# Kernel optimization log

Hardware: AMD Instinct MI355X
Metric: run time of the kernel (lower is better)

The kernel has to match this reference:

```python
import jax, jax.numpy as jnp
import numpy as np

N = 8192
K = 64
EPS = 1e-7
BN_EPS = 1e-5


def _norm(x):
    return jnp.sqrt(jnp.sum(x * x, axis=-1, keepdims=True))


def _bn(x, gamma, beta):
    # BatchNorm2d in training mode (batch statistics, biased variance)
    mu = jnp.mean(x, axis=(0, 2, 3), keepdims=True)
    var = jnp.mean((x - mu) ** 2, axis=(0, 2, 3), keepdims=True)
    return gamma.reshape(1, -1, 1, 1) * (x - mu) / jnp.sqrt(var + BN_EPS) + beta.reshape(1, -1, 1, 1)


def _conv1x1(x, w, b):
    # 1x1 conv == per-pixel linear: x [B,C,H,W], w [O,C]
    return jnp.einsum('bchw,oc->bohw', x, w) + b.reshape(1, -1, 1, 1)


def setup_inputs() -> dict:
    key = jax.random.key(0)
    ks = jax.random.split(key, 24)
    d = {}
    d['points'] = jax.random.normal(ks[0], (1, N, 3), jnp.float32)
    # graph_conv weights (torch code re-draws these every forward; here fixed params)
    lim0 = float(np.sqrt(6.0 / (4 + 64)))
    d['gw0'] = jax.random.uniform(ks[1], (4, 64), jnp.float32, -lim0, lim0)
    lim = float(np.sqrt(6.0 / (64 + 64)))
    for i in range(1, 5):
        d[f'gw{i}'] = jax.random.uniform(ks[1 + i], (64, 64), jnp.float32, -lim, lim)
    # mlp_1: 4->64->128, mlp_2: 192->256->1024 (1x1 convs + BN)
    d['c1w'] = jax.random.normal(ks[6], (64, 4), jnp.float32) * 0.1
    d['c1b'] = jnp.zeros((64,), jnp.float32)
    d['bn1g'] = jnp.ones((64,), jnp.float32)
    d['bn1b'] = jnp.zeros((64,), jnp.float32)
    d['c2w'] = jax.random.normal(ks[7], (128, 64), jnp.float32) * 0.1
    d['c2b'] = jnp.zeros((128,), jnp.float32)
    d['bn2g'] = jnp.ones((128,), jnp.float32)
    d['bn2b'] = jnp.zeros((128,), jnp.float32)
    d['c3w'] = jax.random.normal(ks[8], (256, 192), jnp.float32) * 0.05
    d['c3b'] = jnp.zeros((256,), jnp.float32)
    d['bn3g'] = jnp.ones((256,), jnp.float32)
    d['bn3b'] = jnp.zeros((256,), jnp.float32)
    d['c4w'] = jax.random.normal(ks[9], (1024, 256), jnp.float32) * 0.05
    d['c4b'] = jnp.zeros((1024,), jnp.float32)
    d['bn4g'] = jnp.ones((1024,), jnp.float32)
    d['bn4b'] = jnp.zeros((1024,), jnp.float32)
    return d


def _knn_search(points, k):
    # pairwise squared distances via ||a||^2 - 2ab + ||b||^2
    r = jnp.sum(points * points, axis=-1, keepdims=True)          # [1,N,1]
    dis = r - 2.0 * jnp.einsum('bnd,bmd->bnm', points, points) + jnp.swapaxes(r, 1, 2)
    _, idx = jax.lax.top_k(-dis, k)                                # [1,N,K]
    knn_pts = jax.vmap(lambda p, i: p[i])(points, idx)             # [1,N,K,3]
    return knn_pts


def _proj_knn(knn_pts):
    b, n, k, _ = knn_pts.shape
    pc = knn_pts - knn_pts[:, :, :1, :]                            # center on first neighbor (self)
    vn = jnp.sqrt(jnp.sum(pc * pc, axis=-1))                       # [1,N,K]
    id1 = jnp.argmax(vn, axis=-1)                                  # farthest neighbor
    a1 = jnp.take_along_axis(pc, jnp.broadcast_to(id1[:, :, None, None], (b, n, 1, 3)), axis=2)[:, :, 0, :]
    a1 = a1 / (_norm(a1) + EPS)
    a2 = jnp.mean(pc, axis=2)
    a2 = a2 / (_norm(a2) + EPS)
    a3 = a1 + 1.5 * a2
    a3 = a3 / (_norm(a3) + EPS)
    den = _norm(pc) + EPS                                          # [1,N,K,1]
    f1 = jnp.sum(pc * a1[:, :, None, :], axis=-1, keepdims=True) / den
    f2 = jnp.sum(pc * a2[:, :, None, :], axis=-1, keepdims=True) / den
    f3 = jnp.sum(pc * a3[:, :, None, :], axis=-1, keepdims=True) / den
    return jnp.concatenate([f1, f2, f3, vn[..., None]], axis=-1)   # [1,N,K,4]


def _proj_points(points):
    b, n, _ = points.shape
    vn = jnp.sqrt(jnp.sum(points * points, axis=-1))               # [1,N]
    i1 = jnp.argmax(vn, axis=-1)
    i2 = jnp.argmin(vn, axis=-1)
    a1 = jnp.take_along_axis(points, jnp.broadcast_to(i1[:, None, None], (b, 1, 3)), axis=1)[:, 0, :]
    a1 = a1 / (_norm(a1) + EPS)
    a2 = jnp.take_along_axis(points, jnp.broadcast_to(i2[:, None, None], (b, 1, 3)), axis=1)[:, 0, :]
    a2 = a2 / (_norm(a2) + EPS)
    a3 = a1 + 1.5 * a2
    a3 = a3 / (_norm(a3) + EPS)
    den = _norm(points) + EPS                                      # [1,N,1]
    f1 = jnp.sum(points * a1[:, None, :], axis=-1, keepdims=True) / den
    f2 = jnp.sum(points * a2[:, None, :], axis=-1, keepdims=True) / den
    f3 = jnp.sum(points * a3[:, None, :], axis=-1, keepdims=True) / den
    return jnp.concatenate([f1, f2, f3, vn[..., None]], axis=-1)   # [1,N,4]


def reference(points, gw0, gw1, gw2, gw3, gw4,
              c1w, c1b, bn1g, bn1b, c2w, c2b, bn2g, bn2b,
              c3w, c3b, bn3g, bn3b, c4w, c4b, bn4g, bn4b):
    n = points.shape[1]
    # upper branch: KNN -> rotation-invariant local feats -> 5-layer MLP -> max over K
    knn_pts = _knn_search(points, K)
    feat_up = _proj_knn(knn_pts)                                   # [1,N,K,4]
    x = feat_up.reshape(-1, 4)
    for w in (gw0, gw1, gw2, gw3, gw4):
        x = jax.nn.relu(x @ w)
    x = x.reshape(1, n, K, 64)
    emb_up = jnp.max(x, axis=2, keepdims=True)                     # [1,N,1,64]
    emb_up = emb_up.reshape(1, 64, n, 1)                           # raw view (reshape), as in torch
    # lower branch: global rotation-invariant feats -> mlp_1
    feat_down = _proj_points(points)                               # [1,N,4]
    emb_down = feat_down.reshape(1, 4, n, 1)                       # raw view (reshape), as in torch
    h = jax.nn.relu(_bn(_conv1x1(emb_down, c1w, c1b), bn1g, bn1b))
    h = jax.nn.relu(_bn(_conv1x1(h, c2w, c2b), bn2g, bn2b))        # [1,128,N,1]
    emb = jnp.concatenate([emb_up, h], axis=1)                     # [1,192,N,1]
    out = jax.nn.relu(_bn(_conv1x1(emb, c3w, c3b), bn3g, bn3b))
    out = jax.nn.relu(_bn(_conv1x1(out, c4w, c4b), bn4g, bn4b))    # [1,1024,N,1]
    return out
```

## Files before the change

kernel.cpp:

```cpp
#include <hip/hip_runtime.h>
#include <hip/hip_bf16.h>

#define NPTS 8192
#define KNN 64
#define EPSF 1e-7f

#define OFF_P4      0
#define OFF_STATS   32768
#define OFF_AVEC    36000
#define OFF_PART    36012
#define OFF_FEATDN  36864
#define OFF_WT1     69632
#define OFF_GWT     69888
#define OFF_BW2     79104
#define OFF_BW3     83200
#define OFF_BW4     107776
#define OFF_XB1     238848
#define OFF_XB3     500992
#define OFF_XB4     1287424
#define OFF_Y1      2336000
#define OFF_Y2      2860288
#define OFF_Y3      3908864
#define OFF_FEATUP  6006016

typedef __bf16 bf16x8 __attribute__((ext_vector_type(8)));
typedef float  f32x4  __attribute__((ext_vector_type(4)));

__device__ __forceinline__ unsigned f2u(float f) {
    unsigned u = __float_as_uint(f);
    return ((int)u >= 0) ? (u | 0x80000000u) : ~u;
}
__device__ __forceinline__ float key_to_f(unsigned long long k) {
    unsigned v = (unsigned)(k >> 32);
    unsigned ob = (v & 0x80000000u) ? (v ^ 0x80000000u) : ~v;
    return __uint_as_float(ob);
}
__device__ __forceinline__ unsigned short f2bf(float x) {
    unsigned u = __float_as_uint(x);
    unsigned r = (u + 0x7FFFu + ((u >> 16) & 1u)) >> 16;
    return (unsigned short)r;
}
__device__ __forceinline__ unsigned long long u64min(unsigned long long a, unsigned long long b){ return a < b ? a : b; }
__device__ __forceinline__ unsigned long long u64max(unsigned long long a, unsigned long long b){ return a < b ? b : a; }

__device__ __forceinline__ unsigned long long sort_merge(
    unsigned long long key, unsigned long long cur, int lane)
{
    #pragma unroll
    for (int k = 2; k <= 64; k <<= 1) {
        #pragma unroll
        for (int j = k >> 1; j > 0; j >>= 1) {
            unsigned long long o = __shfl_xor(key, j);
            bool up = ((lane & k) == 0);
            bool lower = ((lane & j) == 0);
            key = (lower == up) ? u64min(key, o) : u64max(key, o);
        }
    }
    unsigned long long rev = __shfl(key, 63 - lane);
    unsigned long long m = u64min(cur, rev);
    #pragma unroll
    for (int j = 32; j > 0; j >>= 1) {
        unsigned long long o = __shfl_xor(m, j);
        m = ((lane & j) == 0) ? u64min(m, o) : u64max(m, o);
    }
    return m;
}

__global__ __launch_bounds__(256) void prep_a_kernel(
    const float* __restrict__ points, float* __restrict__ ws)
{
    const int n = blockIdx.x * 256 + threadIdx.x;
    float x = points[3*n+0], y = points[3*n+1], z = points[3*n+2];
    float rr = x*x + y*y + z*z;
    ((float4*)(ws + OFF_P4))[n] = make_float4(x, y, z, rr);
    float vn = sqrtf(rr);
    unsigned b = __float_as_uint(vn);
    unsigned long long mxk = ((unsigned long long)b << 32) | (unsigned long long)(0xFFFFFFFFu - (unsigned)n);
    unsigned long long mnk = ((unsigned long long)b << 32) | (unsigned long long)(unsigned)n;
    for (int j = 32; j > 0; j >>= 1) {
        mxk = u64max(mxk, __shfl_xor(mxk, j));
        mnk = u64min(mnk, __shfl_xor(mnk, j));
    }
    __shared__ unsigned long long smx[4], smn[4];
    int wid = threadIdx.x >> 6;
    if ((threadIdx.x & 63) == 0) { smx[wid] = mxk; smn[wid] = mnk; }
    __syncthreads();
    if (threadIdx.x == 0) {
        unsigned long long MX = 0ull, MN = ~0ull;
        for (int i = 0; i < 4; ++i) { MX = u64max(MX, smx[i]); MN = u64min(MN, smn[i]); }
        unsigned long long* parts = (unsigned long long*)(ws + OFF_PART);
        parts[2*blockIdx.x + 0] = MX;
        parts[2*blockIdx.x + 1] = MN;
    }
}

__global__ __launch_bounds__(64) void prep_b_kernel(
    const float* __restrict__ points, float* __restrict__ ws)
{
    const int lane = threadIdx.x;
    const unsigned long long* parts = (const unsigned long long*)(ws + OFF_PART);
    unsigned long long mxk = (lane < 32) ? parts[2*lane + 0] : 0ull;
    unsigned long long mnk = (lane < 32) ? parts[2*lane + 1] : ~0ull;
    for (int j = 32; j > 0; j >>= 1) {
        mxk = u64max(mxk, __shfl_xor(mxk, j));
        mnk = u64min(mnk, __shfl_xor(mnk, j));
    }
    if (lane == 0) {
        int i1 = (int)(0xFFFFFFFFu - (unsigned)(mxk & 0xFFFFFFFFu));
        int i2 = (int)(unsigned)(mnk & 0xFFFFFFFFu);
        float a1x = points[3*i1+0], a1y = points[3*i1+1], a1z = points[3*i1+2];
        float n1 = sqrtf(a1x*a1x + a1y*a1y + a1z*a1z) + EPSF;
        a1x /= n1; a1y /= n1; a1z /= n1;
        float a2x = points[3*i2+0], a2y = points[3*i2+1], a2z = points[3*i2+2];
        float n2 = sqrtf(a2x*a2x + a2y*a2y + a2z*a2z) + EPSF;
        a2x /= n2; a2y /= n2; a2z /= n2;
        float a3x = a1x + 1.5f*a2x, a3y = a1y + 1.5f*a2y, a3z = a1z + 1.5f*a2z;
        float n3 = sqrtf(a3x*a3x + a3y*a3y + a3z*a3z) + EPSF;
        a3x /= n3; a3y /= n3; a3z /= n3;
        float* av = ws + OFF_AVEC;
        av[0]=a1x; av[1]=a1y; av[2]=a1z;
        av[3]=a2x; av[4]=a2y; av[5]=a2z;
        av[6]=a3x; av[7]=a3y; av[8]=a3z;
    }
}

__global__ __launch_bounds__(256) void prep_c_kernel(float* __restrict__ ws)
{
    const int n = blockIdx.x * 256 + threadIdx.x;
    const float* av = ws + OFF_AVEC;
    float4 v = ((const float4*)(ws + OFF_P4))[n];
    float vn = sqrtf(v.w);
    float den = vn + EPSF;
    float f1 = (v.x*av[0] + v.y*av[1] + v.z*av[2]) / den;
    float f2 = (v.x*av[3] + v.y*av[4] + v.z*av[5]) / den;
    float f3 = (v.x*av[6] + v.y*av[7] + v.z*av[8]) / den;
    float4* f4 = (float4*)(ws + OFF_FEATDN + 4*n);
    *f4 = make_float4(f1, f2, f3, vn);
}

__global__ __launch_bounds__(256) void wt_kernel(
    const float* __restrict__ c1w, const float* __restrict__ c2w,
    const float* __restrict__ c3w, const float* __restrict__ c4w,
    const float* __restrict__ gw0, const float* __restrict__ gw1,
    const float* __restrict__ gw2, const float* __restrict__ gw3,
    const float* __restrict__ gw4,
    float* __restrict__ ws)
{
    const int t = blockIdx.x * 256 + threadIdx.x;
    const int T = gridDim.x * 256;
    for (int m = t; m < 2944; m += T) ws[OFF_STATS + m] = 0.f;
    for (int m = t; m < 64*4; m += T) { int o = m >> 2, c = m & 3; ws[OFF_WT1 + c*64 + o] = c1w[m]; }

    unsigned short* bw2 = (unsigned short*)(ws + OFF_BW2);
    for (int m = t; m < 128*64; m += T)   bw2[m] = f2bf(c2w[m]);
    unsigned short* bw3 = (unsigned short*)(ws + OFF_BW3);
    for (int m = t; m < 256*192; m += T)  bw3[m] = f2bf(c3w[m]);
    unsigned short* bw4 = (unsigned short*)(ws + OFF_BW4);
    for (int m = t; m < 1024*256; m += T) bw4[m] = f2bf(c4w[m]);

    unsigned short* gwt = (unsigned short*)(ws + OFF_GWT);
    for (int m = t; m < 2048; m += T) {
        int o = m >> 5, i = m & 31;
        gwt[m] = (i < 4) ? f2bf(gw0[i*64 + o]) : (unsigned short)0;
    }
    const float* gsrc[4] = {gw1, gw2, gw3, gw4};
    for (int l = 0; l < 4; ++l) {
        const float* g = gsrc[l];
        unsigned short* dst = gwt + 2048 + l*4096;
        for (int m = t; m < 4096; m += T) { int o = m >> 6, i = m & 63; dst[m] = f2bf(g[i*64 + o]); }
    }
}

__global__ __launch_bounds__(512) void knn_feat_kernel(
    const float4* __restrict__ p4, float4* __restrict__ feat_up)
{
    __shared__ __align__(16) float4 scand[2048];
    __shared__ unsigned long long queue[8][128];
    const int lane = threadIdx.x & 63;
    const int wid  = threadIdx.x >> 6;
    const int q = blockIdx.x * 8 + wid;

    const float4 qa = p4[q];
    unsigned long long cur = ~0ull;
    float kthd = __builtin_inff();
    int qc = 0;
    unsigned long long* Q = queue[wid];

    for (int base = 0; base < NPTS; base += 2048) {
        __syncthreads();
        for (int t = threadIdx.x; t < 2048; t += 512) scand[t] = p4[base + t];
        __syncthreads();
        #pragma unroll 2
        for (int sub = 0; sub < 2048; sub += 64) {
            float4 cd = scand[sub + lane];
            float dot = fmaf(qa.x, cd.x, fmaf(qa.y, cd.y, qa.z * cd.z));
            float d   = fmaf(-2.f, dot, qa.w) + cd.w;
            bool p = d < kthd;
            unsigned long long m = __ballot(p);
            if (m) {
                int prefix = __builtin_amdgcn_mbcnt_hi((unsigned)(m >> 32),
                              __builtin_amdgcn_mbcnt_lo((unsigned)m, 0));
                if (p) Q[qc + prefix] = ((unsigned long long)f2u(d) << 32)
                                      | (unsigned long long)(unsigned)(base + sub + lane);
                qc += __popcll(m);
                if (qc >= 64) {
                    qc -= 64;
                    cur = sort_merge(Q[qc + lane], cur, lane);
                    kthd = key_to_f(__shfl(cur, 63));
                }
            }
        }
    }
    cur = sort_merge((lane < qc) ? Q[lane] : ~0ull, cur, lane);

    int nidx = (int)(unsigned)(cur & 0xFFFFFFFFu);
    float4 np = p4[nidx];
    float ox = __shfl(np.x, 0), oy = __shfl(np.y, 0), oz = __shfl(np.z, 0);
    float pcx = np.x - ox, pcy = np.y - oy, pcz = np.z - oz;
    float vn = sqrtf(pcx*pcx + pcy*pcy + pcz*pcz);

    unsigned long long ak = ((unsigned long long)__float_as_uint(vn) << 32)
                          | (unsigned long long)(unsigned)(63 - lane);
    for (int s = 32; s > 0; s >>= 1) ak = u64max(ak, __shfl_xor(ak, s));
    int id1 = 63 - (int)(unsigned)(ak & 0xFFFFFFFFu);

    float a1x = __shfl(pcx, id1), a1y = __shfl(pcy, id1), a1z = __shfl(pcz, id1);
    float n1 = sqrtf(a1x*a1x + a1y*a1y + a1z*a1z) + EPSF;
    a1x /= n1; a1y /= n1; a1z /= n1;

    float sx = pcx, sy = pcy, sz = pcz;
    for (int s = 32; s > 0; s >>= 1) {
        sx += __shfl_xor(sx, s); sy += __shfl_xor(sy, s); sz += __shfl_xor(sz, s);
    }
    float a2x = sx * (1.f/64.f), a2y = sy * (1.f/64.f), a2z = sz * (1.f/64.f);
    float n2 = sqrtf(a2x*a2x + a2y*a2y + a2z*a2z) + EPSF;
    a2x /= n2; a2y /= n2; a2z /= n2;

    float a3x = a1x + 1.5f*a2x, a3y = a1y + 1.5f*a2y, a3z = a1z + 1.5f*a2z;
    float n3 = sqrtf(a3x*a3x + a3y*a3y + a3z*a3z) + EPSF;
    a3x /= n3; a3y /= n3; a3z /= n3;

    float den = vn + EPSF;
    float f1 = (pcx*a1x + pcy*a1y + pcz*a1z) / den;
    float f2 = (pcx*a2x + pcy*a2y + pcz*a2z) / den;
    float f3 = (pcx*a3x + pcy*a3y + pcz*a3z) / den;
    feat_up[q*64 + lane] = make_float4(f1, f2, f3, vn);
}

#define BROW 72
__global__ __launch_bounds__(256) void mlp_kernel(
    const float4* __restrict__ feat_up,
    const unsigned short* __restrict__ gwt,
    unsigned short* __restrict__ xb3)
{
    __shared__ __align__(16) unsigned short Blds[4][64 * BROW];
    const int lane = threadIdx.x & 63;
    const int wid  = threadIdx.x >> 6;
    const int q = blockIdx.x * 4 + wid;
    const int c = lane & 15, g = lane >> 4;
    unsigned short* B = Blds[wid];

    {
        float4 f = feat_up[q*64 + lane];
        uint2 p0;
        p0.x = (unsigned)f2bf(f.x) | ((unsigned)f2bf(f.y) << 16);
        p0.y = (unsigned)f2bf(f.z) | ((unsigned)f2bf(f.w) << 16);
        *(uint2*)&B[lane*BROW] = p0;
        *(uint2*)&B[lane*BROW + 4] = make_uint2(0, 0);
        uint4 z4 = make_uint4(0, 0, 0, 0);
        *(uint4*)&B[lane*BROW + 8]  = z4;
        *(uint4*)&B[lane*BROW + 16] = z4;
        *(uint4*)&B[lane*BROW + 24] = z4;
    }

    const unsigned short* Wl[5] = {gwt, gwt + 2048, gwt + 6144, gwt + 10240, gwt + 14336};
    f32x4 acc[4][4];

    for (int layer = 0; layer < 5; ++layer) {
        const int wstride = (layer == 0) ? 32 : 64;
        const int nks = (layer == 0) ? 1 : 2;
        #pragma unroll
        for (int mb = 0; mb < 4; ++mb)
            #pragma unroll
            for (int nb = 0; nb < 4; ++nb)
                acc[mb][nb] = (f32x4){0.f, 0.f, 0.f, 0.f};

        for (int ks = 0; ks < nks; ++ks) {
            bf16x8 af[4], bf[4];
            #pragma unroll
            for (int mb = 0; mb < 4; ++mb)
                af[mb] = *(const bf16x8*)(Wl[layer] + (mb*16 + c)*wstride + ks*32 + g*8);
            #pragma unroll
            for (int nb = 0; nb < 4; ++nb)
                bf[nb] = *(const bf16x8*)&B[(nb*16 + c)*BROW + ks*32 + g*8];
            #pragma unroll
            for (int mb = 0; mb < 4; ++mb)
                #pragma unroll
                for (int nb = 0; nb < 4; ++nb)
                    acc[mb][nb] = __builtin_amdgcn_mfma_f32_16x16x32_bf16(af[mb], bf[nb], acc[mb][nb], 0, 0, 0);
        }

        if (layer < 4) {
            #pragma unroll
            for (int mb = 0; mb < 4; ++mb) {
                #pragma unroll
                for (int nb = 0; nb < 4; ++nb) {
                    f32x4 a = acc[mb][nb];
                    float r0 = fmaxf(a[0], 0.f), r1 = fmaxf(a[1], 0.f);
                    float r2 = fmaxf(a[2], 0.f), r3 = fmaxf(a[3], 0.f);
                    uint2 pw;
                    pw.x = (unsigned)f2bf(r0) | ((unsigned)f2bf(r1) << 16);
                    pw.y = (unsigned)f2bf(r2) | ((unsigned)f2bf(r3) << 16);
                    *(uint2*)&B[(nb*16 + c)*BROW + mb*16 + g*4] = pw;
                }
            }
        }
    }

    const int cc = q >> 7;
    const int pbase = (q & 127) << 6;
    #pragma unroll
    for (int mb = 0; mb < 4; ++mb) {
        float v[4];
        #pragma unroll
        for (int r = 0; r < 4; ++r)
            v[r] = fmaxf(fmaxf(fmaxf(acc[mb][0][r], acc[mb][1][r]),
                               fmaxf(acc[mb][2][r], acc[mb][3][r])), 0.f);
        #pragma unroll
        for (int mask = 1; mask <= 8; mask <<= 1)
            #pragma unroll
            for (int r = 0; r < 4; ++r)
                v[r] = fmaxf(v[r], __shfl_xor(v[r], mask));
        if (c == 0) {
            #pragma unroll
            for (int r = 0; r < 4; ++r) {
                const int f = mb*16 + g*4 + r;
                xb3[(size_t)(pbase + f) * 192 + cc] = f2bf(v[r]);
            }
        }
    }
}

__global__ __launch_bounds__(256) void conv1_kernel(
    const float* __restrict__ x, const float* __restrict__ wt,
    const float* __restrict__ bias, float* __restrict__ y,
    float* __restrict__ stout)
{
    const int tid = threadIdx.x;
    const int p  = blockIdx.x * 256 + tid;
    const int o0 = blockIdx.y * 32;
    float acc[32];
    #pragma unroll
    for (int u = 0; u < 32; ++u) acc[u] = bias[o0 + u];
    #pragma unroll
    for (int c = 0; c < 4; ++c) {
        float xv = x[c * NPTS + p];
        const float* wr = wt + c * 64 + o0;
        #pragma unroll
        for (int u = 0; u < 32; ++u) acc[u] = fmaf(xv, wr[u], acc[u]);
    }
    #pragma unroll
    for (int u = 0; u < 32; ++u) y[(o0 + u) * NPTS + p] = acc[u];

    __shared__ float ps[4][32], pss[4][32];
    const int wid = tid >> 6, lane = tid & 63;
    #pragma unroll
    for (int u = 0; u < 32; ++u) {
        float s = acc[u], ss = acc[u] * acc[u];
        for (int j = 32; j > 0; j >>= 1) { s += __shfl_xor(s, j); ss += __shfl_xor(ss, j); }
        if (lane == 0) { ps[wid][u] = s; pss[wid][u] = ss; }
    }
    __syncthreads();
    if (tid < 32) {
        float S  = ps[0][tid] + ps[1][tid] + ps[2][tid] + ps[3][tid];
        float SS = pss[0][tid] + pss[1][tid] + pss[2][tid] + pss[3][tid];
        atomicAdd(&stout[o0 + tid], S);
        atomicAdd(&stout[64 + o0 + tid], SS);
    }
}

__global__ __launch_bounds__(256) void bnpack_kernel(
    const float* __restrict__ y, const float* __restrict__ st,
    const float* __restrict__ gam, const float* __restrict__ bet,
    int C, int stride, int coff, unsigned short* __restrict__ xb)
{
    __shared__ float sc[256], sh[256];
    __shared__ __align__(16) unsigned short tile[64][264];
    const int tid = threadIdx.x;
    for (int cc = tid; cc < C; cc += 256) {
        float mu  = st[cc] * (1.f / 8192.f);
        float var = st[C + cc] * (1.f / 8192.f) - mu * mu;
        float s = gam[cc] / sqrtf(var + 1e-5f);
        sc[cc] = s; sh[cc] = bet[cc] - mu * s;
    }
    __syncthreads();
    const int pl = tid & 63, g = tid >> 6;
    const int p = blockIdx.x * 64 + pl;
    for (int c0 = g * 8; c0 < C; c0 += 32) {
        unsigned pk[4];
        #pragma unroll
        for (int h = 0; h < 4; ++h) {
            float v0 = fmaxf(fmaf(y[(c0 + 2*h    ) * NPTS + p], sc[c0 + 2*h    ], sh[c0 + 2*h    ]), 0.f);
            float v1 = fmaxf(fmaf(y[(c0 + 2*h + 1) * NPTS + p], sc[c0 + 2*h + 1], sh[c0 + 2*h + 1]), 0.f);
            pk[h] = (unsigned)f2bf(v0) | ((unsigned)f2bf(v1) << 16);
        }
        *(uint4*)&tile[pl][c0] = make_uint4(pk[0], pk[1], pk[2], pk[3]);
    }
    __syncthreads();
    const int cpr = C >> 3;
    const int nch = 64 * cpr;
    for (int idx = tid; idx < nch; idx += 256) {
        int r = idx / cpr, cc = (idx - r * cpr) * 8;
        *(uint4*)&xb[(size_t)(blockIdx.x * 64 + r) * stride + coff + cc] = *(uint4*)&tile[r][cc];
    }
}

__global__ __launch_bounds__(256) void conv_mfma_kernel(
    const unsigned short* __restrict__ A, const unsigned short* __restrict__ Bx,
    const float* __restrict__ bias, int K, int M,
    float* __restrict__ y, float* __restrict__ stout)
{
    const int lane = threadIdx.x & 63;
    const int w = threadIdx.x >> 6;
    const int n0 = blockIdx.x * 256 + w * 64;
    const int m0 = blockIdx.y * 64;
    const int c = lane & 15, g = lane >> 4;

    f32x4 acc[4][4];
    #pragma unroll
    for (int mt = 0; mt < 4; ++mt)
        #pragma unroll
        for (int nt = 0; nt < 4; ++nt)
            acc[mt][nt] = (f32x4){0.f, 0.f, 0.f, 0.f};

    for (int k0 = 0; k0 < K; k0 += 32) {
        bf16x8 af[4], bf[4];
        #pragma unroll
        for (int mt = 0; mt < 4; ++mt)
            af[mt] = *(const bf16x8*)(A + (size_t)(m0 + mt*16 + c) * K + k0 + g*8);
        #pragma unroll
        for (int nt = 0; nt < 4; ++nt)
            bf[nt] = *(const bf16x8*)(Bx + (size_t)(n0 + nt*16 + c) * K + k0 + g*8);
        #pragma unroll
        for (int mt = 0; mt < 4; ++mt)
            #pragma unroll
            for (int nt = 0; nt < 4; ++nt)
                acc[mt][nt] = __builtin_amdgcn_mfma_f32_16x16x32_bf16(af[mt], bf[nt], acc[mt][nt], 0, 0, 0);
    }

    #pragma unroll
    for (int mt = 0; mt < 4; ++mt) {
        float s[4], ss[4];
        #pragma unroll
        for (int r = 0; r < 4; ++r) {
            const int o = m0 + mt*16 + g*4 + r;
            const float bv = bias[o];
            float sum = 0.f, sq = 0.f;
            #pragma unroll
            for (int nt = 0; nt < 4; ++nt) {
                float v = acc[mt][nt][r] + bv;
                y[(size_t)o * NPTS + n0 + nt*16 + c] = v;
                sum += v; sq += v * v;
            }
            s[r] = sum; ss[r] = sq;
        }
        #pragma unroll
        for (int mask = 1; mask <= 8; mask <<= 1)
            #pragma unroll
            for (int r = 0; r < 4; ++r) {
                s[r]  += __shfl_xor(s[r],  mask);
                ss[r] += __shfl_xor(ss[r], mask);
            }
        if (c == 0) {
            #pragma unroll
            for (int r = 0; r < 4; ++r) {
                const int o = m0 + mt*16 + g*4 + r;
                atomicAdd(&stout[o], s[r]);
                atomicAdd(&stout[M + o], ss[r]);
            }
        }
    }
}

__global__ __launch_bounds__(256) void bnrelu_kernel(
    const float4* y, const float* __restrict__ st,
    const float* __restrict__ g, const float* __restrict__ b,
    float4* out, int C)
{
    int idx = blockIdx.x * 256 + threadIdx.x;
    int c = idx >> 11;
    float mu  = st[c] * (1.f / 8192.f);
    float var = st[C + c] * (1.f / 8192.f) - mu * mu;
    float scale = g[c] / sqrtf(var + 1e-5f);
    float sh = b[c] - mu * scale;
    float4 v = y[idx];
    v.x = fmaxf(fmaf(v.x, scale, sh), 0.f);
    v.y = fmaxf(fmaf(v.y, scale, sh), 0.f);
    v.z = fmaxf(fmaf(v.z, scale, sh), 0.f);
    v.w = fmaxf(fmaf(v.w, scale, sh), 0.f);
    out[idx] = v;
}

extern "C" void kernel_launch(void* const* d_in, const int* in_sizes, int n_in,
                              void* d_out, int out_size, void* d_ws, size_t ws_size,
                              hipStream_t stream) {
    const float* points = (const float*)d_in[0];
    const float* gw0 = (const float*)d_in[1];
    const float* gw1 = (const float*)d_in[2];
    const float* gw2 = (const float*)d_in[3];
    const float* gw3 = (const float*)d_in[4];
    const float* gw4 = (const float*)d_in[5];
    const float* c1w = (const float*)d_in[6];  const float* c1b = (const float*)d_in[7];
    const float* bn1g = (const float*)d_in[8]; const float* bn1b = (const float*)d_in[9];
    const float* c2w = (const float*)d_in[10]; const float* c2b = (const float*)d_in[11];
    const float* bn2g = (const float*)d_in[12];const float* bn2b = (const float*)d_in[13];
    const float* c3w = (const float*)d_in[14]; const float* c3b = (const float*)d_in[15];
    const float* bn3g = (const float*)d_in[16];const float* bn3b = (const float*)d_in[17];
    const float* c4w = (const float*)d_in[18]; const float* c4b = (const float*)d_in[19];
    const float* bn4g = (const float*)d_in[20];const float* bn4b = (const float*)d_in[21];

    float* ws = (float*)d_ws;
    float* p4f    = ws + OFF_P4;
    float* featdn = ws + OFF_FEATDN;
    float* featup = ws + OFF_FEATUP;
    float* y1 = ws + OFF_Y1; float* y2 = ws + OFF_Y2; float* y3 = ws + OFF_Y3;
    float* s1 = ws + OFF_STATS + 0;
    float* s2 = ws + OFF_STATS + 128;
    float* s3 = ws + OFF_STATS + 384;
    float* s4 = ws + OFF_STATS + 896;
    float* wt1 = ws + OFF_WT1;
    const unsigned short* gwt = (const unsigned short*)(ws + OFF_GWT);
    const unsigned short* bw2 = (const unsigned short*)(ws + OFF_BW2);
    const unsigned short* bw3 = (const unsigned short*)(ws + OFF_BW3);
    const unsigned short* bw4 = (const unsigned short*)(ws + OFF_BW4);
    unsigned short* xb1 = (unsigned short*)(ws + OFF_XB1);
    unsigned short* xb3 = (unsigned short*)(ws + OFF_XB3);
    unsigned short* xb4 = (unsigned short*)(ws + OFF_XB4);
    float* outp = (float*)d_out;

    prep_a_kernel<<<32, 256, 0, stream>>>(points, ws);
    prep_b_kernel<<<1, 64, 0, stream>>>(points, ws);
    prep_c_kernel<<<32, 256, 0, stream>>>(ws);
    wt_kernel<<<256, 256, 0, stream>>>(c1w, c2w, c3w, c4w, gw0, gw1, gw2, gw3, gw4, ws);

    knn_feat_kernel<<<1024, 512, 0, stream>>>((const float4*)p4f, (float4*)featup);
    mlp_kernel<<<2048, 256, 0, stream>>>((const float4*)featup, gwt, xb3);

    conv1_kernel<<<dim3(32, 2), 256, 0, stream>>>(featdn, wt1, c1b, y1, s1);
    bnpack_kernel<<<128, 256, 0, stream>>>(y1, s1, bn1g, bn1b, 64, 64, 0, xb1);
    conv_mfma_kernel<<<dim3(32, 2), 256, 0, stream>>>(bw2, xb1, c2b, 64, 128, y2, s2);
    bnpack_kernel<<<128, 256, 0, stream>>>(y2, s2, bn2g, bn2b, 128, 192, 64, xb3);
    conv_mfma_kernel<<<dim3(32, 4), 256, 0, stream>>>(bw3, xb3, c3b, 192, 256, y3, s3);
    bnpack_kernel<<<128, 256, 0, stream>>>(y3, s3, bn3g, bn3b, 256, 256, 0, xb4);
    conv_mfma_kernel<<<dim3(32, 16), 256, 0, stream>>>(bw4, xb4, c4b, 256, 1024, outp, s4);
    bnrelu_kernel<<<8192, 256, 0, stream>>>((const float4*)outp, s4, bn4g, bn4b, (float4*)outp, 1024);
}
```

Before: 354.9 us.

## Derive final BN stats from input Gram matrix and fuse BN-ReLU into conv4

Computes the layer-4 batch-norm mean and variance analytically from the 256x256 Gram matrix of the bf16 input, plus per-channel input sums, instead of from the 1024xN conv output. The last conv can then apply BN and ReLU in its epilogue, so the separate read-modify-write pass over the 32MB output goes away. It also merges the prep and weight kernels into one launch and staggers the KNN candidate order per wave. The cost is a transposed copy of the activations, written with strided scattered stores in bnpack, a serial 8192-long Gram kernel on only 64 blocks, and possible precision differences in the variance.

```diff
diff --git a/kernel.cpp b/kernel.cpp
--- a/kernel.cpp
+++ b/kernel.cpp
@@ -7,7 +7,6 @@
 
 #define OFF_P4      0
 #define OFF_STATS   32768
-#define OFF_AVEC    36000
 #define OFF_PART    36012
 #define OFF_FEATDN  36864
 #define OFF_WT1     69632
@@ -22,6 +21,11 @@
 #define OFF_Y2      2860288
 #define OFF_Y3      3908864
 #define OFF_FEATUP  6006016
+#define OFF_S4      OFF_Y1
+#define OFF_MSUM    (OFF_Y1 + 65536)
+#define OFF_SC4     (OFF_Y1 + 65792)
+#define OFF_SH4     (OFF_Y1 + 66816)
+#define OFF_XB4T    OFF_Y2
 
 typedef __bf16 bf16x8 __attribute__((ext_vector_type(8)));
 typedef float  f32x4  __attribute__((ext_vector_type(4)));
@@ -39,6 +43,9 @@
     unsigned u = __float_as_uint(x);
     unsigned r = (u + 0x7FFFu + ((u >> 16) & 1u)) >> 16;
     return (unsigned short)r;
+}
+__device__ __forceinline__ float bf2f(unsigned short u) {
+    return __uint_as_float((unsigned)u << 16);
 }
 __device__ __forceinline__ unsigned long long u64min(unsigned long long a, unsigned long long b){ return a < b ? a : b; }
 __device__ __forceinline__ unsigned long long u64max(unsigned long long a, unsigned long long b){ return a < b ? b : a; }
@@ -66,68 +73,97 @@
     return m;
 }
 
-__global__ __launch_bounds__(256) void prep_a_kernel(
-    const float* __restrict__ points, float* __restrict__ ws)
-{
-    const int n = blockIdx.x * 256 + threadIdx.x;
-    float x = points[3*n+0], y = points[3*n+1], z = points[3*n+2];
-    float rr = x*x + y*y + z*z;
-    ((float4*)(ws + OFF_P4))[n] = make_float4(x, y, z, rr);
-    float vn = sqrtf(rr);
-    unsigned b = __float_as_uint(vn);
-    unsigned long long mxk = ((unsigned long long)b << 32) | (unsigned long long)(0xFFFFFFFFu - (unsigned)n);
-    unsigned long long mnk = ((unsigned long long)b << 32) | (unsigned long long)(unsigned)n;
-    for (int j = 32; j > 0; j >>= 1) {
-        mxk = u64max(mxk, __shfl_xor(mxk, j));
-        mnk = u64min(mnk, __shfl_xor(mnk, j));
-    }
-    __shared__ unsigned long long smx[4], smn[4];
-    int wid = threadIdx.x >> 6;
-    if ((threadIdx.x & 63) == 0) { smx[wid] = mxk; smn[wid] = mnk; }
+__global__ __launch_bounds__(256) void prepwt_kernel(
+    const float* __restrict__ points,
+    const float* __restrict__ c1w, const float* __restrict__ c2w,
+    const float* __restrict__ c3w, const float* __restrict__ c4w,
+    const float* __restrict__ gw0, const float* __restrict__ gw1,
+    const float* __restrict__ gw2, const float* __restrict__ gw3,
+    const float* __restrict__ gw4,
+    float* __restrict__ ws)
+{
+    const int t = blockIdx.x * 256 + threadIdx.x;
+    const int T = 256 * 256;
+    for (int m = t; m < 2944; m += T) ws[OFF_STATS + m] = 0.f;
+    for (int m = t; m < 64*4; m += T) { int o = m >> 2, c = m & 3; ws[OFF_WT1 + c*64 + o] = c1w[m]; }
+
+    unsigned short* bw2 = (unsigned short*)(ws + OFF_BW2);
+    for (int m = t; m < 128*64; m += T)   bw2[m] = f2bf(c2w[m]);
+    unsigned short* bw3 = (unsigned short*)(ws + OFF_BW3);
+    for (int m = t; m < 256*192; m += T)  bw3[m] = f2bf(c3w[m]);
+    unsigned short* bw4 = (unsigned short*)(ws + OFF_BW4);
+    for (int m = t; m < 1024*256; m += T) bw4[m] = f2bf(c4w[m]);
+
+    unsigned short* gwt = (unsigned short*)(ws + OFF_GWT);
+    for (int m = t; m < 2048; m += T) {
+        int o = m >> 5, i = m & 31;
+        gwt[m] = (i < 4) ? f2bf(gw0[i*64 + o]) : (unsigned short)0;
+    }
+    const float* gsrc[4] = {gw1, gw2, gw3, gw4};
+    for (int l = 0; l < 4; ++l) {
+        const float* g = gsrc[l];
+        unsigned short* dst = gwt + 2048 + l*4096;
+        for (int m = t; m < 4096; m += T) { int o = m >> 6, i = m & 63; dst[m] = f2bf(g[i*64 + o]); }
+    }
+
+    if (blockIdx.x < 32) {
+        const int n = blockIdx.x * 256 + threadIdx.x;
+        float x = points[3*n+0], y = points[3*n+1], z = points[3*n+2];
+        float rr = x*x + y*y + z*z;
+        ((float4*)(ws + OFF_P4))[n] = make_float4(x, y, z, rr);
+        float vn = sqrtf(rr);
+        unsigned b = __float_as_uint(vn);
+        unsigned long long mxk = ((unsigned long long)b << 32) | (unsigned long long)(0xFFFFFFFFu - (unsigned)n);
+        unsigned long long mnk = ((unsigned long long)b << 32) | (unsigned long long)(unsigned)n;
+        for (int j = 32; j > 0; j >>= 1) {
+            mxk = u64max(mxk, __shfl_xor(mxk, j));
+            mnk = u64min(mnk, __shfl_xor(mnk, j));
+        }
+        __shared__ unsigned long long smx[4], smn[4];
+        int wid = threadIdx.x >> 6;
+        if ((threadIdx.x & 63) == 0) { smx[wid] = mxk; smn[wid] = mnk; }
+        __syncthreads();
+        if (threadIdx.x == 0) {
+            unsigned long long MX = 0ull, MN = ~0ull;
+            for (int i = 0; i < 4; ++i) { MX = u64max(MX, smx[i]); MN = u64min(MN, smn[i]); }
+            unsigned long long* parts = (unsigned long long*)(ws + OFF_PART);
+            parts[2*blockIdx.x + 0] = MX;
+            parts[2*blockIdx.x + 1] = MN;
+        }
+    }
+}
+
+__global__ __launch_bounds__(256) void prep_c_kernel(float* __restrict__ ws)
+{
+    __shared__ float av[9];
+    const int tid = threadIdx.x;
+    if (tid < 64) {
+        const unsigned long long* parts = (const unsigned long long*)(ws + OFF_PART);
+        unsigned long long mxk = (tid < 32) ? parts[2*tid + 0] : 0ull;
+        unsigned long long mnk = (tid < 32) ? parts[2*tid + 1] : ~0ull;
+        for (int j = 32; j > 0; j >>= 1) {
+            mxk = u64max(mxk, __shfl_xor(mxk, j));
+            mnk = u64min(mnk, __shfl_xor(mnk, j));
+        }
+        if (tid == 0) {
+            int i1 = (int)(0xFFFFFFFFu - (unsigned)(mxk & 0xFFFFFFFFu));
+            int i2 = (int)(unsigned)(mnk & 0xFFFFFFFFu);
+            float4 p1 = ((const float4*)(ws + OFF_P4))[i1];
+            float4 p2 = ((const float4*)(ws + OFF_P4))[i2];
+            float n1 = sqrtf(p1.x*p1.x + p1.y*p1.y + p1.z*p1.z) + EPSF;
+            float a1x = p1.x/n1, a1y = p1.y/n1, a1z = p1.z/n1;
+            float n2 = sqrtf(p2.x*p2.x + p2.y*p2.y + p2.z*p2.z) + EPSF;
+            float a2x = p2.x/n2, a2y = p2.y/n2, a2z = p2.z/n2;
+            float a3x = a1x + 1.5f*a2x, a3y = a1y + 1.5f*a2y, a3z = a1z + 1.5f*a2z;
+            float n3 = sqrtf(a3x*a3x + a3y*a3y + a3z*a3z) + EPSF;
+            a3x /= n3; a3y /= n3; a3z /= n3;
+            av[0]=a1x; av[1]=a1y; av[2]=a1z;
+            av[3]=a2x; av[4]=a2y; av[5]=a2z;
+            av[6]=a3x; av[7]=a3y; av[8]=a3z;
+        }
+    }
     __syncthreads();
-    if (threadIdx.x == 0) {
-        unsigned long long MX = 0ull, MN = ~0ull;
-        for (int i = 0; i < 4; ++i) { MX = u64max(MX, smx[i]); MN = u64min(MN, smn[i]); }
-        unsigned long long* parts = (unsigned long long*)(ws + OFF_PART);
-        parts[2*blockIdx.x + 0] = MX;
-        parts[2*blockIdx.x + 1] = MN;
-    }
-}
-
-__global__ __launch_bounds__(64) void prep_b_kernel(
-    const float* __restrict__ points, float* __restrict__ ws)
-{
-    const int lane = threadIdx.x;
-    const unsigned long long* parts = (const unsigned long long*)(ws + OFF_PART);
-    unsigned long long mxk = (lane < 32) ? parts[2*lane + 0] : 0ull;
-    unsigned long long mnk = (lane < 32) ? parts[2*lane + 1] : ~0ull;
-    for (int j = 32; j > 0; j >>= 1) {
-        mxk = u64max(mxk, __shfl_xor(mxk, j));
-        mnk = u64min(mnk, __shfl_xor(mnk, j));
-    }
-    if (lane == 0) {
-        int i1 = (int)(0xFFFFFFFFu - (unsigned)(mxk & 0xFFFFFFFFu));
-        int i2 = (int)(unsigned)(mnk & 0xFFFFFFFFu);
-        float a1x = points[3*i1+0], a1y = points[3*i1+1], a1z = points[3*i1+2];
-        float n1 = sqrtf(a1x*a1x + a1y*a1y + a1z*a1z) + EPSF;
-        a1x /= n1; a1y /= n1; a1z /= n1;
-        float a2x = points[3*i2+0], a2y = points[3*i2+1], a2z = points[3*i2+2];
-        float n2 = sqrtf(a2x*a2x + a2y*a2y + a2z*a2z) + EPSF;
-        a2x /= n2; a2y /= n2; a2z /= n2;
-        float a3x = a1x + 1.5f*a2x, a3y = a1y + 1.5f*a2y, a3z = a1z + 1.5f*a2z;
-        float n3 = sqrtf(a3x*a3x + a3y*a3y + a3z*a3z) + EPSF;
-        a3x /= n3; a3y /= n3; a3z /= n3;
-        float* av = ws + OFF_AVEC;
-        av[0]=a1x; av[1]=a1y; av[2]=a1z;
-        av[3]=a2x; av[4]=a2y; av[5]=a2z;
-        av[6]=a3x; av[7]=a3y; av[8]=a3z;
-    }
-}
-
-__global__ __launch_bounds__(256) void prep_c_kernel(float* __restrict__ ws)
-{
-    const int n = blockIdx.x * 256 + threadIdx.x;
-    const float* av = ws + OFF_AVEC;
+    const int n = blockIdx.x * 256 + tid;
     float4 v = ((const float4*)(ws + OFF_P4))[n];
     float vn = sqrtf(v.w);
     float den = vn + EPSF;
@@ -138,39 +174,6 @@
     *f4 = make_float4(f1, f2, f3, vn);
 }
 
-__global__ __launch_bounds__(256) void wt_kernel(
-    const float* __restrict__ c1w, const float* __restrict__ c2w,
-    const float* __restrict__ c3w, const float* __restrict__ c4w,
-    const float* __restrict__ gw0, const float* __restrict__ gw1,
-    const float* __restrict__ gw2, const float* __restrict__ gw3,
-    const float* __restrict__ gw4,
-    float* __restrict__ ws)
-{
-    const int t = blockIdx.x * 256 + threadIdx.x;
-    const int T = gridDim.x * 256;
-    for (int m = t; m < 2944; m += T) ws[OFF_STATS + m] = 0.f;
-    for (int m = t; m < 64*4; m += T) { int o = m >> 2, c = m & 3; ws[OFF_WT1 + c*64 + o] = c1w[m]; }
-
-    unsigned short* bw2 = (unsigned short*)(ws + OFF_BW2);
-    for (int m = t; m < 128*64; m += T)   bw2[m] = f2bf(c2w[m]);
-    unsigned short* bw3 = (unsigned short*)(ws + OFF_BW3);
-    for (int m = t; m < 256*192; m += T)  bw3[m] = f2bf(c3w[m]);
-    unsigned short* bw4 = (unsigned short*)(ws + OFF_BW4);
-    for (int m = t; m < 1024*256; m += T) bw4[m] = f2bf(c4w[m]);
-
-    unsigned short* gwt = (unsigned short*)(ws + OFF_GWT);
-    for (int m = t; m < 2048; m += T) {
-        int o = m >> 5, i = m & 31;
-        gwt[m] = (i < 4) ? f2bf(gw0[i*64 + o]) : (unsigned short)0;
-    }
-    const float* gsrc[4] = {gw1, gw2, gw3, gw4};
-    for (int l = 0; l < 4; ++l) {
-        const float* g = gsrc[l];
-        unsigned short* dst = gwt + 2048 + l*4096;
-        for (int m = t; m < 4096; m += T) { int o = m >> 6, i = m & 63; dst[m] = f2bf(g[i*64 + o]); }
-    }
-}
-
 __global__ __launch_bounds__(512) void knn_feat_kernel(
     const float4* __restrict__ p4, float4* __restrict__ feat_up)
 {
@@ -191,7 +194,8 @@
         for (int t = threadIdx.x; t < 2048; t += 512) scand[t] = p4[base + t];
         __syncthreads();
         #pragma unroll 2
-        for (int sub = 0; sub < 2048; sub += 64) {
+        for (int s = 0; s < 32; ++s) {
+            const int sub = ((s + wid * 4) & 31) << 6;
             float4 cd = scand[sub + lane];
             float dot = fmaf(qa.x, cd.x, fmaf(qa.y, cd.y, qa.z * cd.z));
             float d   = fmaf(-2.f, dot, qa.w) + cd.w;
@@ -382,7 +386,8 @@
 __global__ __launch_bounds__(256) void bnpack_kernel(
     const float* __restrict__ y, const float* __restrict__ st,
     const float* __restrict__ gam, const float* __restrict__ bet,
-    int C, int stride, int coff, unsigned short* __restrict__ xb)
+    int C, int stride, int coff, unsigned short* __restrict__ xb,
+    unsigned short* __restrict__ xt)
 {
     __shared__ float sc[256], sh[256];
     __shared__ __align__(16) unsigned short tile[64][264];
@@ -405,6 +410,13 @@
             pk[h] = (unsigned)f2bf(v0) | ((unsigned)f2bf(v1) << 16);
         }
         *(uint4*)&tile[pl][c0] = make_uint4(pk[0], pk[1], pk[2], pk[3]);
+        if (xt) {
+            #pragma unroll
+            for (int h = 0; h < 4; ++h) {
+                xt[(size_t)(c0 + 2*h    ) * NPTS + p] = (unsigned short)(pk[h] & 0xFFFFu);
+                xt[(size_t)(c0 + 2*h + 1) * NPTS + p] = (unsigned short)(pk[h] >> 16);
+            }
+        }
     }
     __syncthreads();
     const int cpr = C >> 3;
@@ -482,23 +494,143 @@
     }
 }
 
-__global__ __launch_bounds__(256) void bnrelu_kernel(
-    const float4* y, const float* __restrict__ st,
-    const float* __restrict__ g, const float* __restrict__ b,
-    float4* out, int C)
-{
-    int idx = blockIdx.x * 256 + threadIdx.x;
-    int c = idx >> 11;
-    float mu  = st[c] * (1.f / 8192.f);
-    float var = st[C + c] * (1.f / 8192.f) - mu * mu;
-    float scale = g[c] / sqrtf(var + 1e-5f);
-    float sh = b[c] - mu * scale;
-    float4 v = y[idx];
-    v.x = fmaxf(fmaf(v.x, scale, sh), 0.f);
-    v.y = fmaxf(fmaf(v.y, scale, sh), 0.f);
-    v.z = fmaxf(fmaf(v.z, scale, sh), 0.f);
-    v.w = fmaxf(fmaf(v.w, scale, sh), 0.f);
-    out[idx] = v;
+__global__ __launch_bounds__(256) void gram4_kernel(
+    const unsigned short* __restrict__ Xt,
+    float* __restrict__ S, float* __restrict__ msum)
+{
+    const int lane = threadIdx.x & 63;
+    const int w = threadIdx.x >> 6;
+    const int mt = w >> 1, nt = w & 1;
+    const int m0 = blockIdx.x * 32 + mt * 16;
+    const int n1 = blockIdx.y * 32 + nt * 16;
+    const int c = lane & 15, g = lane >> 4;
+    const bool domsum = (blockIdx.y == 0) && (nt == 0);
+
+    f32x4 acc = (f32x4){0.f, 0.f, 0.f, 0.f};
+    float ms = 0.f;
+    const unsigned short* arow = Xt + (size_t)(m0 + c) * NPTS;
+    const unsigned short* brow = Xt + (size_t)(n1 + c) * NPTS;
+    for (int k0 = 0; k0 < NPTS; k0 += 32) {
+        bf16x8 af = *(const bf16x8*)(arow + k0 + g*8);
+        bf16x8 bf = *(const bf16x8*)(brow + k0 + g*8);
+        acc = __builtin_amdgcn_mfma_f32_16x16x32_bf16(af, bf, acc, 0, 0, 0);
+        if (domsum) {
+            const unsigned short* ap = (const unsigned short*)&af;
+            #pragma unroll
+            for (int e = 0; e < 8; ++e) ms += bf2f(ap[e]);
+        }
+    }
+    #pragma unroll
+    for (int r = 0; r < 4; ++r)
+        S[(size_t)(m0 + g*4 + r) * 256 + n1 + c] = acc[r];
+    if (domsum) {
+        ms += __shfl_xor(ms, 16);
+        ms += __shfl_xor(ms, 32);
+        if (g == 0) msum[m0 + c] = ms;
+    }
+}
+
+__global__ __launch_bounds__(256) void solve4_kernel(
+    const float* __restrict__ S, const float* __restrict__ msum,
+    const unsigned short* __restrict__ w4, const float* __restrict__ bias,
+    const float* __restrict__ gam, const float* __restrict__ bet,
+    float* __restrict__ sc, float* __restrict__ sh)
+{
+    __shared__ float wf[8][256];
+    const int tid = threadIdx.x;
+    const int ob = blockIdx.x * 8;
+    for (int m = tid; m < 8 * 256; m += 256) {
+        int oo = m >> 8, j = m & 255;
+        wf[oo][j] = bf2f(w4[(size_t)(ob + oo) * 256 + j]);
+    }
+    __syncthreads();
+    const int lane = tid & 63, w = tid >> 6;
+    const int jj = lane * 4;
+    float4 wA = *(const float4*)&wf[w*2+0][jj];
+    float4 wB = *(const float4*)&wf[w*2+1][jj];
+    float ta0=0.f, ta1=0.f, ta2=0.f, ta3=0.f;
+    float tb0=0.f, tb1=0.f, tb2=0.f, tb3=0.f;
+    for (int i = 0; i < 256; ++i) {
+        float4 sv = ((const float4*)(S + (size_t)i * 256))[lane];
+        float wia = wf[w*2+0][i];
+        float wib = wf[w*2+1][i];
+        ta0 = fmaf(sv.x, wia, ta0); ta1 = fmaf(sv.y, wia, ta1);
+        ta2 = fmaf(sv.z, wia, ta2); ta3 = fmaf(sv.w, wia, ta3);
+        tb0 = fmaf(sv.x, wib, tb0); tb1 = fmaf(sv.y, wib, tb1);
+        tb2 = fmaf(sv.z, wib, tb2); tb3 = fmaf(sv.w, wib, tb3);
+    }
+    float4 m4 = ((const float4*)msum)[lane];
+    float qa = ta0*wA.x + ta1*wA.y + ta2*wA.z + ta3*wA.w;
+    float qb = tb0*wB.x + tb1*wB.y + tb2*wB.z + tb3*wB.w;
+    float ma = m4.x*wA.x + m4.y*wA.y + m4.z*wA.z + m4.w*wA.w;
+    float mb = m4.x*wB.x + m4.y*wB.y + m4.z*wB.z + m4.w*wB.w;
+    for (int j = 32; j > 0; j >>= 1) {
+        qa += __shfl_xor(qa, j); qb += __shfl_xor(qb, j);
+        ma += __shfl_xor(ma, j); mb += __shfl_xor(mb, j);
+    }
+    if (lane == 0) {
+        const float invN = 1.f / 8192.f;
+        int oA = ob + w*2, oB = oA + 1;
+        float mdA = ma * invN, mdB = mb * invN;
+        float muA = mdA + bias[oA], muB = mdB + bias[oB];
+        float varA = qa * invN - mdA * mdA;
+        float varB = qb * invN - mdB * mdB;
+        float scA = gam[oA] / sqrtf(varA + 1e-5f);
+        float scB = gam[oB] / sqrtf(varB + 1e-5f);
+        sc[oA] = scA; sh[oA] = bet[oA] - muA * scA;
+        sc[oB] = scB; sh[oB] = bet[oB] - muB * scB;
+    }
+}
+
+__global__ __launch_bounds__(256) void conv4bn_kernel(
+    const unsigned short* __restrict__ A, const unsigned short* __restrict__ Bx,
+    const float* __restrict__ bias, int K, int M,
+    const float* __restrict__ sc, const float* __restrict__ sh,
+    float* __restrict__ out)
+{
+    const int lane = threadIdx.x & 63;
+    const int w = threadIdx.x >> 6;
+    const int n0 = blockIdx.x * 256 + w * 64;
+    const int m0 = blockIdx.y * 64;
+    const int c = lane & 15, g = lane >> 4;
+
+    f32x4 acc[4][4];
+    #pragma unroll
+    for (int mt = 0; mt < 4; ++mt)
+        #pragma unroll
+        for (int nt = 0; nt < 4; ++nt)
+            acc[mt][nt] = (f32x4){0.f, 0.f, 0.f, 0.f};
+
+    for (int k0 = 0; k0 < K; k0 += 32) {
+        bf16x8 af[4], bf[4];
+        #pragma unroll
+        for (int mt = 0; mt < 4; ++mt)
+            af[mt] = *(const bf16x8*)(A + (size_t)(m0 + mt*16 + c) * K + k0 + g*8);
+        #pragma unroll
+        for (int nt = 0; nt < 4; ++nt)
+            bf[nt] = *(const bf16x8*)(Bx + (size_t)(n0 + nt*16 + c) * K + k0 + g*8);
+        #pragma unroll
+        for (int mt = 0; mt < 4; ++mt)
+            #pragma unroll
+            for (int nt = 0; nt < 4; ++nt)
+                acc[mt][nt] = __builtin_amdgcn_mfma_f32_16x16x32_bf16(af[mt], bf[nt], acc[mt][nt], 0, 0, 0);
+    }
+
+    #pragma unroll
+    for (int mt = 0; mt < 4; ++mt) {
+        #pragma unroll
+        for (int r = 0; r < 4; ++r) {
+            const int o = m0 + mt*16 + g*4 + r;
+            const float bv = bias[o];
+            const float s = sc[o];
+            const float h = sh[o];
+            #pragma unroll
+            for (int nt = 0; nt < 4; ++nt) {
+                float v = acc[mt][nt][r] + bv;
+                out[(size_t)o * NPTS + n0 + nt*16 + c] = fmaxf(fmaf(v, s, h), 0.f);
+            }
+        }
+    }
 }
 
 extern "C" void kernel_launch(void* const* d_in, const int* in_sizes, int n_in,
@@ -527,7 +659,6 @@
     float* s1 = ws + OFF_STATS + 0;
     float* s2 = ws + OFF_STATS + 128;
     float* s3 = ws + OFF_STATS + 384;
-    float* s4 = ws + OFF_STATS + 896;
     float* wt1 = ws + OFF_WT1;
     const unsigned short* gwt = (const unsigned short*)(ws + OFF_GWT);
     const unsigned short* bw2 = (const unsigned short*)(ws + OFF_BW2);
@@ -536,22 +667,27 @@
     unsigned short* xb1 = (unsigned short*)(ws + OFF_XB1);
     unsigned short* xb3 = (unsigned short*)(ws + OFF_XB3);
     unsigned short* xb4 = (unsigned short*)(ws + OFF_XB4);
+    unsigned short* xb4t = (unsigned short*)(ws + OFF_XB4T);
+    float* S4   = ws + OFF_S4;
+    float* msum = ws + OFF_MSUM;
+    float* sc4  = ws + OFF_SC4;
+    float* sh4  = ws + OFF_SH4;
     float* outp = (float*)d_out;
 
-    prep_a_kernel<<<32, 256, 0, stream>>>(points, ws);
-    prep_b_kernel<<<1, 64, 0, stream>>>(points, ws);
+    prepwt_kernel<<<256, 256, 0, stream>>>(points, c1w, c2w, c3w, c4w,
+                                           gw0, gw1, gw2, gw3, gw4, ws);
     prep_c_kernel<<<32, 256, 0, stream>>>(ws);
-    wt_kernel<<<256, 256, 0, stream>>>(c1w, c2w, c3w, c4w, gw0, gw1, gw2, gw3, gw4, ws);
 
     knn_feat_kernel<<<1024, 512, 0, stream>>>((const float4*)p4f, (float4*)featup);
     mlp_kernel<<<2048, 256, 0, stream>>>((const float4*)featup, gwt, xb3);
 
     conv1_kernel<<<dim3(32, 2), 256, 0, stream>>>(featdn, wt1, c1b, y1, s1);
-    bnpack_kernel<<<128, 256, 0, stream>>>(y1, s1, bn1g, bn1b, 64, 64, 0, xb1);
+    bnpack_kernel<<<128, 256, 0, stream>>>(y1, s1, bn1g, bn1b, 64, 64, 0, xb1, nullptr);
     conv_mfma_kernel<<<dim3(32, 2), 256, 0, stream>>>(bw2, xb1, c2b, 64, 128, y2, s2);
-    bnpack_kernel<<<128, 256, 0, stream>>>(y2, s2, bn2g, bn2b, 128, 192, 64, xb3);
+    bnpack_kernel<<<128, 256, 0, stream>>>(y2, s2, bn2g, bn2b, 128, 192, 64, xb3, nullptr);
     conv_mfma_kernel<<<dim3(32, 4), 256, 0, stream>>>(bw3, xb3, c3b, 192, 256, y3, s3);
-    bnpack_kernel<<<128, 256, 0, stream>>>(y3, s3, bn3g, bn3b, 256, 256, 0, xb4);
-    conv_mfma_kernel<<<dim3(32, 16), 256, 0, stream>>>(bw4, xb4, c4b, 256, 1024, outp, s4);
-    bnrelu_kernel<<<8192, 256, 0, stream>>>((const float4*)outp, s4, bn4g, bn4b, (float4*)outp, 1024);
-}
+    bnpack_kernel<<<128, 256, 0, stream>>>(y3, s3, bn3g, bn3b, 256, 256, 0, xb4, xb4t);
+    gram4_kernel<<<dim3(8, 8), 256, 0, stream>>>(xb4t, S4, msum);
+    solve4_kernel<<<128, 256, 0, stream>>>(S4, msum, bw4, c4b, bn4g, bn4b, sc4, sh4);
+    conv4bn_kernel<<<dim3(32, 16), 256, 0, stream>>>(bw4, xb4, c4b, 256, 1024, sc4, sh4, outp);
+}
```

Result: slower. 420.8 us (+18.6%).
